# Performance work log

Hardware: AMD Instinct MI355X
Metric: run time of the kernel (lower is better)

## Reference

```python
import jax, jax.numpy as jnp
import numpy as np

V, D, C, B, S, H = 50000, 256, 10, 64, 512, 512


def setup_inputs() -> dict:
    key = jax.random.key(0)
    ks = jax.random.split(key, 12)
    s = 0.02
    return {
        "x": jax.random.randint(ks[0], (B, S), 0, V),
        "embed_w": jax.random.normal(ks[1], (V, D), dtype=jnp.float32) * s,
        "Wl": jax.random.normal(ks[2], (D, D), dtype=jnp.float32) * s,
        "bl": jnp.zeros((D,), jnp.float32),
        "Wsl": jax.random.normal(ks[3], (D, D), dtype=jnp.float32) * s,
        "bsl": jnp.zeros((D,), jnp.float32),
        "Wr": jax.random.normal(ks[4], (D, D), dtype=jnp.float32) * s,
        "br": jnp.zeros((D,), jnp.float32),
        "Wsr": jax.random.normal(ks[5], (D, D), dtype=jnp.float32) * s,
        "bsr": jnp.zeros((D,), jnp.float32),
        "conv_w": jax.random.normal(ks[6], (H, 3 * D), dtype=jnp.float32) * s,
        "conv_b": jnp.zeros((H,), jnp.float32),
        "fc_w": jax.random.normal(ks[7], (C, H), dtype=jnp.float32) * s,
        "fc_b": jnp.zeros((C,), jnp.float32),
        "cl0": jax.random.normal(ks[8], (B, D), dtype=jnp.float32),
        "cr0": jax.random.normal(ks[9], (B, D), dtype=jnp.float32),
    }


def reference(x, embed_w, Wl, bl, Wsl, bsl, Wr, br, Wsr, bsr,
              conv_w, conv_b, fc_w, fc_b, cl0, cr0):
    e = embed_w[x]  # [B,S,D] embedding lookup
    # Precompute the embedding-dependent half of each recurrence (one big GEMM)
    pre_l = jnp.swapaxes(jnp.einsum("bsd,ed->bse", e, Wsl) + bsl, 0, 1)  # [S,B,D]
    pre_r = jnp.swapaxes(jnp.einsum("bsd,ed->bse", e, Wsr) + bsr, 0, 1)  # [S,B,D]

    # left[0]=cl0; left[t]=relu(Wl left[t-1] + Wsl e[t-1])  (output carry, then update)
    def lstep(c, p):
        return jax.nn.relu(c @ Wl.T + bl + p), c

    _, left = jax.lax.scan(lstep, cl0, pre_l)  # [S,B,D]

    # right[S-1]=cr0; right[t]=relu(Wr right[t+1] + Wsr e[t+1])
    def rstep(c, p):
        return jax.nn.relu(c @ Wr.T + br + p), c

    _, right = jax.lax.scan(rstep, cr0, pre_r, reverse=True)  # [S,B,D]

    ctx = jnp.concatenate(
        [jnp.swapaxes(left, 0, 1), e, jnp.swapaxes(right, 0, 1)], axis=-1
    )  # [B,S,3D]
    # Conv2d(1,512,(1,3D)) == per-timestep linear 3D->512
    h = jax.nn.relu(jnp.einsum("bsd,hd->bsh", ctx, conv_w) + conv_b)  # [B,S,H]
    pooled = h.max(axis=1)  # max_pool1d over full sequence -> [B,H]
    return pooled @ fc_w.T + fc_b  # [B,C]
```

## Files before the change

### kernel.cpp

```cpp
#include <hip/hip_runtime.h>
#include <hip/hip_bf16.h>

#define VOCAB 50000
#define DD 256
#define NCLS 10
#define BB 64
#define SS 512
#define HH 512
#define K3D 768

typedef __attribute__((ext_vector_type(8))) short bf16x8;
typedef __attribute__((ext_vector_type(8))) unsigned short ush8;
typedef __attribute__((ext_vector_type(4))) float f32x4;

static __device__ __forceinline__ unsigned short f2bf(float f) {
    __hip_bfloat16 h = __float2bfloat16(f);
    return *reinterpret_cast<unsigned short*>(&h);
}

static __device__ __forceinline__ ush8 cvt8(const float* src) {
    const float4 lo = *(const float4*)(src);
    const float4 hi = *(const float4*)(src + 4);
    uint4 u;
    asm("v_cvt_pk_bf16_f32 %0, %1, %2" : "=v"(u.x) : "v"(lo.x), "v"(lo.y));
    asm("v_cvt_pk_bf16_f32 %0, %1, %2" : "=v"(u.y) : "v"(lo.z), "v"(lo.w));
    asm("v_cvt_pk_bf16_f32 %0, %1, %2" : "=v"(u.z) : "v"(hi.x), "v"(hi.y));
    asm("v_cvt_pk_bf16_f32 %0, %1, %2" : "=v"(u.w) : "v"(hi.z), "v"(hi.w));
    return *reinterpret_cast<ush8*>(&u);
}

#define PPAD 72

__global__ __launch_bounds__(256) void prep_pre_kernel(
    const float* __restrict__ Wsl, const float* __restrict__ Wsr,
    const float* __restrict__ bsl, const float* __restrict__ bl,
    const float* __restrict__ bsr, const float* __restrict__ br,
    const int* __restrict__ x, const float* __restrict__ embed_w,
    const float* __restrict__ conv_w,
    unsigned short* __restrict__ convwb,
    float* __restrict__ pre2_l, float* __restrict__ pre2_r,
    float* __restrict__ pooled)
{
    __shared__ unsigned short Abuf[2][128][PPAD];
    __shared__ unsigned short Bbuf[2][128][PPAD];
    __shared__ int xs[128];

    const int bid = blockIdx.x;
    const int tid = threadIdx.x;

    if (bid < 1024) {
        const int mi  = bid & 3;
        const int sbi = bid >> 2;
        const int w = tid >> 6, lane = tid & 63;
        const int lr = lane & 15, g = lane >> 4;
        const int lk = g * 8;
        const int strow = tid >> 3;
        const int skc   = (tid & 7) * 8;

        if (tid < 128)
            xs[tid] = x[(tid & 63) * SS + 2 * sbi + (tid >> 6)];

        f32x4 acc[2][8];
#pragma unroll
        for (int mt = 0; mt < 2; ++mt)
#pragma unroll
            for (int nt = 0; nt < 8; ++nt) acc[mt][nt] = (f32x4)(0.f);

        auto stage = [&](int ks, int buf) {
            const int k0 = ks * 64;
#pragma unroll
            for (int j = 0; j < 4; ++j) {
                const int row = strow + 32 * j;
                const float* wsrc = (mi < 2 ? Wsl + (size_t)(mi * 128 + row) * DD
                                            : Wsr + (size_t)((mi - 2) * 128 + row) * DD)
                                    + k0 + skc;
                *(ush8*)&Abuf[buf][row][skc] = cvt8(wsrc);
                const float* esrc = embed_w + (size_t)xs[row] * DD + k0 + skc;
                *(ush8*)&Bbuf[buf][row][skc] = cvt8(esrc);
            }
        };

        __syncthreads();
        stage(0, 0);
        int cur = 0;
        for (int ks = 0; ks < 4; ++ks) {
            __syncthreads();
            if (ks + 1 < 4) stage(ks + 1, cur ^ 1);
#pragma unroll
            for (int k2 = 0; k2 < 2; ++k2) {
                const int kk = k2 * 32 + lk;
                const bf16x8 a0 = *(const bf16x8*)&Abuf[cur][w * 32 + lr][kk];
                const bf16x8 a1 = *(const bf16x8*)&Abuf[cur][w * 32 + 16 + lr][kk];
#pragma unroll
                for (int nt = 0; nt < 8; ++nt) {
                    const bf16x8 bv = *(const bf16x8*)&Bbuf[cur][nt * 16 + lr][kk];
                    acc[0][nt] = __builtin_amdgcn_mfma_f32_16x16x32_bf16(a0, bv, acc[0][nt], 0, 0, 0);
                    acc[1][nt] = __builtin_amdgcn_mfma_f32_16x16x32_bf16(a1, bv, acc[1][nt], 0, 0, 0);
                }
            }
            cur ^= 1;
        }

#pragma unroll
        for (int mt = 0; mt < 2; ++mt) {
            const int eg = mi * 128 + w * 32 + mt * 16 + g * 4;
            const int e  = eg & 255;
            const float* bsx = (eg < 256) ? bsl : bsr;
            const float* bbx = (eg < 256) ? bl  : br;
            const float4 b1 = *(const float4*)(bsx + e);
            const float4 b2 = *(const float4*)(bbx + e);
            float* dstb = (eg >= 256) ? pre2_r : pre2_l;
#pragma unroll
            for (int nt = 0; nt < 8; ++nt) {
                const int sb = sbi * 128 + nt * 16 + lr;
                const int s = sb >> 6, bgq = (sb >> 4) & 3, b_loc = sb & 15;
                float4 v;
                v.x = acc[mt][nt][0] + b1.x + b2.x;
                v.y = acc[mt][nt][1] + b1.y + b2.y;
                v.z = acc[mt][nt][2] + b1.z + b2.z;
                v.w = acc[mt][nt][3] + b1.w + b2.w;
                *(float4*)(dstb + ((size_t)s * 4 + bgq) * 4096 + (e >> 2) * 64 + b_loc * 4) = v;
            }
        }
    } else if (bid < 1216) {
        const int g = (bid - 1024) * 256 + tid;
        *(ush8*)(convwb + (size_t)g * 8) = cvt8(conv_w + (size_t)g * 8);
    } else {
        float4* p = (float4*)pooled;
#pragma unroll
        for (int i = 0; i < 32; ++i)
            p[tid + 256 * i] = make_float4(0.f, 0.f, 0.f, 0.f);
    }
}

#define CSWZ(row, off) ((off) ^ (((row) & 15) << 4))
#define APAD 72

__global__ __launch_bounds__(256, 1) void recur_conve_kernel(
    const float* __restrict__ Wl, const float* __restrict__ Wr,
    const float* __restrict__ cl0, const float* __restrict__ cr0,
    const float* __restrict__ pre2_l, const float* __restrict__ pre2_r,
    unsigned short* __restrict__ outl, unsigned short* __restrict__ outr,
    const int* __restrict__ x, const float* __restrict__ embed_w,
    const unsigned short* __restrict__ convwb,
    unsigned short* __restrict__ hpart)
{
    __shared__ alignas(16) unsigned char smem[2 * 2 * 128 * APAD * 2];
    __shared__ int xsv[512];

    const int tid  = threadIdx.x;
    const int lane = tid & 63;

    if (blockIdx.x < 8) {
        unsigned short* cbf0 = (unsigned short*)smem;
        unsigned short* cbf1 = (unsigned short*)smem + 16 * 256;

        const int dir = blockIdx.x >> 2;
        const int bg  = blockIdx.x & 3;
        const int b0  = bg * 16;
        const int wl  = tid >> 6;
        const int col = lane & 15;
        const int g   = lane >> 4;

        const float* W   = dir ? Wr : Wl;
        const float* c0  = dir ? cr0 : cl0;
        const float* pre = dir ? pre2_r : pre2_l;
        unsigned short* out = dir ? outr : outl;

        bf16x8 wfrag[4][8];
#pragma unroll
        for (int mt = 0; mt < 4; ++mt)
#pragma unroll
            for (int i = 0; i < 8; ++i) {
                const int kt = (i + 2 * wl) & 7;
                const float* src = W + (size_t)(wl * 64 + mt * 16 + col) * DD
                                     + kt * 32 + g * 8;
                const ush8 p = cvt8(src);
                wfrag[mt][i] = *(bf16x8*)&p;
            }

        int soff[8];
#pragma unroll
        for (int i = 0; i < 8; ++i) {
            const int kt = (i + 2 * wl) & 7;
            soff[i] = CSWZ(col, kt * 64 + g * 16);
        }

        {
            const int blc = tid >> 4;
            const int ch  = tid & 15;
            const float* src = c0 + (size_t)(b0 + blc) * DD + ch * 16;
            const ush8 p0 = cvt8(src);
            const ush8 p1 = cvt8(src + 8);
            char* rowp = (char*)cbf0 + blc * 512;
            *(ush8*)(rowp + CSWZ(blc, ch * 32))      = p0;
            *(ush8*)(rowp + CSWZ(blc, ch * 32 + 16)) = p1;
            const int t0 = dir ? 511 : 0;
            ush8* dst = (ush8*)(out + ((size_t)t0 * BB + b0 + blc) * DD + ch * 16);
            dst[0] = p0; dst[1] = p1;
        }

        const int lpre = (wl * 16 + g) * 64 + col * 4;
        const ptrdiff_t pstep = dir ? -(ptrdiff_t)16384 : (ptrdiff_t)16384;
        const float* p0 = pre + ((size_t)(dir ? 511 : 0) * 4 + bg) * 4096 + lpre;

        float4 pA0 = *(const float4*)(p0);
        float4 pA1 = *(const float4*)(p0 + 256);
        float4 pA2 = *(const float4*)(p0 + 512);
        float4 pA3 = *(const float4*)(p0 + 768);
        const float* p1p = p0 + pstep;
        float4 pB0 = *(const float4*)(p1p);
        float4 pB1 = *(const float4*)(p1p + 256);
        float4 pB2 = *(const float4*)(p1p + 512);
        float4 pB3 = *(const float4*)(p1p + 768);
        const float* pfetch = p0 + 2 * pstep;

        unsigned short* oplane = out + (size_t)(dir ? 510 : 1) * BB * DD
                                     + (b0 + col) * DD + wl * 64 + g * 4;
        const ptrdiff_t ostep = (dir ? -(ptrdiff_t)1 : (ptrdiff_t)1) * (BB * DD);

        __syncthreads();

        int cur = 0;
#pragma unroll 2
        for (int k = 0; k < SS - 1; ++k) {
            bf16x8 sfrag[8];
            {
                const char* rowp = (const char*)(cur ? cbf1 : cbf0) + col * 512;
#pragma unroll
                for (int i = 0; i < 8; ++i)
                    sfrag[i] = *(const bf16x8*)(rowp + soff[i]);
            }

            const float4 pN0 = *(const float4*)(pfetch);
            const float4 pN1 = *(const float4*)(pfetch + 256);
            const float4 pN2 = *(const float4*)(pfetch + 512);
            const float4 pN3 = *(const float4*)(pfetch + 768);
            if (k < SS - 4) pfetch += pstep;

            char* nbuf = (char*)(cur ? cbf0 : cbf1) + col * 512;

            auto epi = [&](int mt, const f32x4 a) {
                const float v0 = fmaxf(a[0], 0.f);
                const float v1 = fmaxf(a[1], 0.f);
                const float v2 = fmaxf(a[2], 0.f);
                const float v3 = fmaxf(a[3], 0.f);
                uint2 uu;
                asm("v_cvt_pk_bf16_f32 %0, %1, %2" : "=v"(uu.x) : "v"(v0), "v"(v1));
                asm("v_cvt_pk_bf16_f32 %0, %1, %2" : "=v"(uu.y) : "v"(v2), "v"(v3));
                const int eoff = (wl * 64 + mt * 16 + g * 4) * 2;
                *(uint2*)(nbuf + CSWZ(col, eoff)) = uu;
                *(uint2*)(oplane + mt * 16) = uu;
            };

            f32x4 a0 = *(const f32x4*)&pA0;
            f32x4 a1 = *(const f32x4*)&pA1;
            __builtin_amdgcn_s_setprio(1);
#pragma unroll
            for (int i = 0; i < 8; ++i) {
                a0 = __builtin_amdgcn_mfma_f32_16x16x32_bf16(wfrag[0][i], sfrag[i], a0, 0, 0, 0);
                a1 = __builtin_amdgcn_mfma_f32_16x16x32_bf16(wfrag[1][i], sfrag[i], a1, 0, 0, 0);
            }
            __builtin_amdgcn_s_setprio(0);
            epi(0, a0);
            epi(1, a1);

            f32x4 a2 = *(const f32x4*)&pA2;
            f32x4 a3 = *(const f32x4*)&pA3;
            __builtin_amdgcn_s_setprio(1);
#pragma unroll
            for (int i = 0; i < 8; ++i) {
                a2 = __builtin_amdgcn_mfma_f32_16x16x32_bf16(wfrag[2][i], sfrag[i], a2, 0, 0, 0);
                a3 = __builtin_amdgcn_mfma_f32_16x16x32_bf16(wfrag[3][i], sfrag[i], a3, 0, 0, 0);
            }
            __builtin_amdgcn_s_setprio(0);
            epi(2, a2);
            epi(3, a3);

            pA0 = pB0; pA1 = pB1; pA2 = pB2; pA3 = pB3;
            pB0 = pN0; pB1 = pN1; pB2 = pN2; pB3 = pN3;
            oplane += ostep;

            asm volatile("s_waitcnt lgkmcnt(0)" ::: "memory");
            __builtin_amdgcn_s_barrier();
            asm volatile("" ::: "memory");
            cur ^= 1;
        }
        return;
    }

    unsigned short* Ab = (unsigned short*)smem;
    unsigned short* Bb = (unsigned short*)smem + 2 * 128 * APAD;

    const int wid = tid >> 6;
    const int lr  = lane & 15;
    const int lk  = (lane >> 4) * 8;
    const int strow = tid >> 3;
    const int skc   = (tid & 7) * 8;

    for (int rep = 0; rep < 2; ++rep) {
        const int cid = (blockIdx.x - 8) + rep * 128;
        const int b   = cid >> 2;
        const int h0  = (cid & 3) * 128;

        for (int i = tid; i < SS; i += 256) xsv[i] = x[b * SS + i];
        __syncthreads();

        f32x4 acc[2][8];
#pragma unroll
        for (int st = 0; st < 2; ++st)
#pragma unroll
            for (int ht = 0; ht < 8; ++ht) acc[st][ht] = (f32x4)(0.f);

        auto stage = [&](int it, int buf) {
            const int stile = it >> 2, kstep = it & 3;
            const int k0 = kstep * 64;
            const int s0 = stile * 128;
#pragma unroll
            for (int j = 0; j < 4; ++j) {
                const int row = strow + 32 * j;
                const int ss = s0 + row;
                const float* esrc = embed_w + (size_t)xsv[ss] * DD + k0 + skc;
                *(ush8*)&Ab[(buf * 128 + row) * APAD + skc] = cvt8(esrc);
                *(bf16x8*)&Bb[(buf * 128 + row) * APAD + skc] =
                    *(const bf16x8*)(convwb + (size_t)(h0 + row) * K3D + 256 + k0 + skc);
            }
        };

        stage(0, 0);
        int cur = 0;
        for (int it = 0; it < 16; ++it) {
            __syncthreads();
            if (it + 1 < 16) stage(it + 1, cur ^ 1);

            const int wrow0 = wid * 32;
#pragma unroll
            for (int ks = 0; ks < 2; ++ks) {
                const int kk = ks * 32 + lk;
                const bf16x8 a0 = *(const bf16x8*)&Ab[(cur * 128 + wrow0 + lr) * APAD + kk];
                const bf16x8 a1 = *(const bf16x8*)&Ab[(cur * 128 + wrow0 + 16 + lr) * APAD + kk];
#pragma unroll
                for (int ht = 0; ht < 8; ++ht) {
                    const bf16x8 bv = *(const bf16x8*)&Bb[(cur * 128 + ht * 16 + lr) * APAD + kk];
                    acc[0][ht] = __builtin_amdgcn_mfma_f32_16x16x32_bf16(a0, bv, acc[0][ht], 0, 0, 0);
                    acc[1][ht] = __builtin_amdgcn_mfma_f32_16x16x32_bf16(a1, bv, acc[1][ht], 0, 0, 0);
                }
            }
            if ((it & 3) == 3) {
                const int stile = it >> 2;
                unsigned short* hp = hpart + (size_t)(cid * 4 + stile) * 16384;
#pragma unroll
                for (int st = 0; st < 2; ++st)
#pragma unroll
                    for (int ht = 0; ht < 8; ++ht) {
                        uint2 uu;
                        asm("v_cvt_pk_bf16_f32 %0, %1, %2"
                            : "=v"(uu.x) : "v"(acc[st][ht][0]), "v"(acc[st][ht][1]));
                        asm("v_cvt_pk_bf16_f32 %0, %1, %2"
                            : "=v"(uu.y) : "v"(acc[st][ht][2]), "v"(acc[st][ht][3]));
                        const int f = (wid * 2 + st) * 8 + ht;
                        *(uint2*)(hp + f * 256 + lane * 4) = uu;
                        acc[st][ht] = (f32x4)(0.f);
                    }
            }
            cur ^= 1;
        }
        __syncthreads();
    }
}

#define KSTEP 64
#define NKC 8

__global__ __launch_bounds__(256) void conv_pool_kernel(
    const unsigned short* __restrict__ leftb,
    const unsigned short* __restrict__ rightb,
    const unsigned short* __restrict__ convwb,
    const unsigned short* __restrict__ hpart,
    const float* __restrict__ conv_b,
    float* __restrict__ pooled)
{
    __shared__ unsigned short Abuf[2][128][APAD];
    __shared__ unsigned short Bbuf[2][128][APAD];
    __shared__ float red[4][128];

    const int stile = blockIdx.x & 3;
    const int h0i   = (blockIdx.x >> 2) & 3;
    const int b     = blockIdx.x >> 4;
    const int h0    = h0i * 128;
    const int s0    = stile * 128;
    const int tid = threadIdx.x;
    const int wid = tid >> 6;
    const int lane = tid & 63;
    const int lr  = lane & 15;
    const int lk  = (lane >> 4) * 8;
    const int strow = tid >> 3;
    const int skc   = (tid & 7) * 8;

    f32x4 acc[2][8];
    {
        const unsigned short* hp = hpart
            + ((size_t)((b * 4 + h0i) * 4 + stile)) * 16384;
#pragma unroll
        for (int st = 0; st < 2; ++st)
#pragma unroll
            for (int ht = 0; ht < 8; ++ht) {
                const int f = (wid * 2 + st) * 8 + ht;
                const uint2 uu = *(const uint2*)(hp + f * 256 + lane * 4);
                f32x4 v;
                v[0] = __uint_as_float(uu.x << 16);
                v[1] = __uint_as_float(uu.x & 0xffff0000u);
                v[2] = __uint_as_float(uu.y << 16);
                v[3] = __uint_as_float(uu.y & 0xffff0000u);
                acc[st][ht] = v;
            }
    }

    auto stage = [&](int kstep, int buf) {
        const int k0 = kstep * KSTEP;
        const unsigned short* asrc;
        int koff, bcol;
        if (k0 < DD) { asrc = leftb;  koff = k0;      bcol = k0; }
        else         { asrc = rightb; koff = k0 - DD; bcol = k0 + 256; }
#pragma unroll
        for (int j = 0; j < 4; ++j) {
            const int row = strow + 32 * j;
            const int ss = s0 + row;
            *(bf16x8*)&Abuf[buf][row][skc] =
                *(const bf16x8*)(asrc + ((size_t)ss * BB + b) * DD + koff + skc);
            *(bf16x8*)&Bbuf[buf][row][skc] =
                *(const bf16x8*)(convwb + (size_t)(h0 + row) * K3D + bcol + skc);
        }
    };

    stage(0, 0);
    int cur = 0;
    for (int it = 0; it < NKC; ++it) {
        __syncthreads();
        if (it + 1 < NKC) stage(it + 1, cur ^ 1);

        const int wrow0 = wid * 32;
#pragma unroll
        for (int ks = 0; ks < 2; ++ks) {
            const int kk = ks * 32 + lk;
            const bf16x8 a0 = *(const bf16x8*)&Abuf[cur][wrow0 + lr][kk];
            const bf16x8 a1 = *(const bf16x8*)&Abuf[cur][wrow0 + 16 + lr][kk];
#pragma unroll
            for (int ht = 0; ht < 8; ++ht) {
                const bf16x8 bv = *(const bf16x8*)&Bbuf[cur][ht * 16 + lr][kk];
                acc[0][ht] = __builtin_amdgcn_mfma_f32_16x16x32_bf16(a0, bv, acc[0][ht], 0, 0, 0);
                acc[1][ht] = __builtin_amdgcn_mfma_f32_16x16x32_bf16(a1, bv, acc[1][ht], 0, 0, 0);
            }
        }
        cur ^= 1;
    }

    float pmax[8];
#pragma unroll
    for (int ht = 0; ht < 8; ++ht) {
        float m = -INFINITY;
#pragma unroll
        for (int st = 0; st < 2; ++st)
#pragma unroll
            for (int r = 0; r < 4; ++r)
                m = fmaxf(m, acc[st][ht][r]);
        m = fmaxf(m, __shfl_xor(m, 16));
        m = fmaxf(m, __shfl_xor(m, 32));
        if (lane < 16) red[wid][ht * 16 + lane] = m;
    }
    __syncthreads();
    if (tid < 128) {
        const float m = fmaxf(fmaxf(red[0][tid], red[1][tid]),
                              fmaxf(red[2][tid], red[3][tid]));
        const float v = fmaxf(m + conv_b[h0 + tid], 0.f);
        atomicMax((unsigned*)(pooled + (size_t)b * HH + h0 + tid),
                  __float_as_uint(v));
    }
}

__global__ void fc_kernel(const float* __restrict__ pooled,
                          const float* __restrict__ fc_w,
                          const float* __restrict__ fc_b,
                          float* __restrict__ out)
{
    const int t = threadIdx.x;
    if (t >= BB * NCLS) return;
    const int b = t / NCLS, c = t % NCLS;
    float acc = fc_b[c];
    for (int h = 0; h < HH; ++h)
        acc += pooled[(size_t)b * HH + h] * fc_w[(size_t)c * HH + h];
    out[b * NCLS + c] = acc;
}

extern "C" void kernel_launch(void* const* d_in, const int* in_sizes, int n_in,
                              void* d_out, int out_size, void* d_ws, size_t ws_size,
                              hipStream_t stream)
{
    const int*   x       = (const int*)  d_in[0];
    const float* embed_w = (const float*)d_in[1];
    const float* Wl      = (const float*)d_in[2];
    const float* bl      = (const float*)d_in[3];
    const float* Wsl     = (const float*)d_in[4];
    const float* bsl     = (const float*)d_in[5];
    const float* Wr      = (const float*)d_in[6];
    const float* br      = (const float*)d_in[7];
    const float* Wsr     = (const float*)d_in[8];
    const float* bsr     = (const float*)d_in[9];
    const float* conv_w  = (const float*)d_in[10];
    const float* conv_b  = (const float*)d_in[11];
    const float* fc_w    = (const float*)d_in[12];
    const float* fc_b    = (const float*)d_in[13];
    const float* cl0     = (const float*)d_in[14];
    const float* cr0     = (const float*)d_in[15];
    float* out = (float*)d_out;

    char* ws = (char*)d_ws;
    const size_t SZf = (size_t)SS * BB * DD * sizeof(float);
    const size_t SZh = (size_t)SS * BB * DD * sizeof(unsigned short);
    float*          pre2_l = (float*)(ws);
    float*          pre2_r = (float*)(ws + SZf);
    unsigned short* leftb  = (unsigned short*)(ws + 2 * SZf);
    unsigned short* rightb = (unsigned short*)(ws + 2 * SZf + SZh);
    unsigned short* convwb = (unsigned short*)(ws + 2 * SZf + 2 * SZh);
    float*          pooled = (float*)(ws + 2 * SZf + 2 * SZh + (size_t)HH * K3D * 2);
    unsigned short* hpart  = (unsigned short*)(ws + 2 * SZf + 2 * SZh
                                               + (size_t)HH * K3D * 2
                                               + (size_t)BB * HH * 4);

    prep_pre_kernel<<<1217, 256, 0, stream>>>(
        Wsl, Wsr, bsl, bl, bsr, br, x, embed_w, conv_w,
        convwb, pre2_l, pre2_r, pooled);

    recur_conve_kernel<<<136, 256, 0, stream>>>(
        Wl, Wr, cl0, cr0, pre2_l, pre2_r, leftb, rightb,
        x, embed_w, convwb, hpart);

    conv_pool_kernel<<<1024, 256, 0, stream>>>(
        leftb, rightb, convwb, hpart, conv_b, pooled);

    fc_kernel<<<1, BB * NCLS, 0, stream>>>(pooled, fc_w, fc_b, out);
}
```

Baseline: 426.0 us.

## Overlap pre-activation GEMM with recurrence using per-timestep readiness counters

Moves the embedding-projection GEMM into the same launch as the recurrence. GEMM blocks publish completion through per-step atomic counters and are ordered from both sequence ends, so each recurrence block can start as soon as its next timesteps are ready instead of waiting for the whole GEMM kernel. The aim is to hide the GEMM time and one kernel boundary behind the serial recurrence. The cost is spin-waiting on global atomics, which relies on the recurrence blocks (low block indices) being scheduled alongside the GEMM blocks and risks stalls if block dispatch order is not guaranteed.

```diff
diff --git a/kernel.cpp b/kernel.cpp
--- a/kernel.cpp
+++ b/kernel.cpp
@@ -29,123 +29,43 @@
     return *reinterpret_cast<ush8*>(&u);
 }
 
-#define PPAD 72
-
-__global__ __launch_bounds__(256) void prep_pre_kernel(
+__global__ __launch_bounds__(256) void prep_small_kernel(
+    const float* __restrict__ conv_w,
+    unsigned short* __restrict__ convwb,
+    float* __restrict__ pooled,
+    int* __restrict__ cnt)
+{
+    const int bid = blockIdx.x;
+    const int tid = threadIdx.x;
+    if (bid < 192) {
+        const int g = bid * 256 + tid;
+        *(ush8*)(convwb + (size_t)g * 8) = cvt8(conv_w + (size_t)g * 8);
+    } else {
+        float4* p = (float4*)pooled;
+#pragma unroll
+        for (int i = 0; i < 32; ++i)
+            p[tid + 256 * i] = make_float4(0.f, 0.f, 0.f, 0.f);
+        if (tid < 128) ((int4*)cnt)[tid] = make_int4(0, 0, 0, 0);
+    }
+}
+
+#define CSWZ(row, off) ((off) ^ (((row) & 15) << 4))
+#define APAD 72
+
+__global__ __launch_bounds__(256, 1) void recur_pre_conve_kernel(
+    const float* __restrict__ Wl, const float* __restrict__ Wr,
+    const float* __restrict__ cl0, const float* __restrict__ cr0,
     const float* __restrict__ Wsl, const float* __restrict__ Wsr,
     const float* __restrict__ bsl, const float* __restrict__ bl,
     const float* __restrict__ bsr, const float* __restrict__ br,
     const int* __restrict__ x, const float* __restrict__ embed_w,
-    const float* __restrict__ conv_w,
-    unsigned short* __restrict__ convwb,
     float* __restrict__ pre2_l, float* __restrict__ pre2_r,
-    float* __restrict__ pooled)
+    unsigned short* __restrict__ outl, unsigned short* __restrict__ outr,
+    const unsigned short* __restrict__ convwb,
+    unsigned short* __restrict__ hpart,
+    int* __restrict__ cnt)
 {
-    __shared__ unsigned short Abuf[2][128][PPAD];
-    __shared__ unsigned short Bbuf[2][128][PPAD];
-    __shared__ int xs[128];
-
-    const int bid = blockIdx.x;
-    const int tid = threadIdx.x;
-
-    if (bid < 1024) {
-        const int mi  = bid & 3;
-        const int sbi = bid >> 2;
-        const int w = tid >> 6, lane = tid & 63;
-        const int lr = lane & 15, g = lane >> 4;
-        const int lk = g * 8;
-        const int strow = tid >> 3;
-        const int skc   = (tid & 7) * 8;
-
-        if (tid < 128)
-            xs[tid] = x[(tid & 63) * SS + 2 * sbi + (tid >> 6)];
-
-        f32x4 acc[2][8];
-#pragma unroll
-        for (int mt = 0; mt < 2; ++mt)
-#pragma unroll
-            for (int nt = 0; nt < 8; ++nt) acc[mt][nt] = (f32x4)(0.f);
-
-        auto stage = [&](int ks, int buf) {
-            const int k0 = ks * 64;
-#pragma unroll
-            for (int j = 0; j < 4; ++j) {
-                const int row = strow + 32 * j;
-                const float* wsrc = (mi < 2 ? Wsl + (size_t)(mi * 128 + row) * DD
-                                            : Wsr + (size_t)((mi - 2) * 128 + row) * DD)
-                                    + k0 + skc;
-                *(ush8*)&Abuf[buf][row][skc] = cvt8(wsrc);
-                const float* esrc = embed_w + (size_t)xs[row] * DD + k0 + skc;
-                *(ush8*)&Bbuf[buf][row][skc] = cvt8(esrc);
-            }
-        };
-
-        __syncthreads();
-        stage(0, 0);
-        int cur = 0;
-        for (int ks = 0; ks < 4; ++ks) {
-            __syncthreads();
-            if (ks + 1 < 4) stage(ks + 1, cur ^ 1);
-#pragma unroll
-            for (int k2 = 0; k2 < 2; ++k2) {
-                const int kk = k2 * 32 + lk;
-                const bf16x8 a0 = *(const bf16x8*)&Abuf[cur][w * 32 + lr][kk];
-                const bf16x8 a1 = *(const bf16x8*)&Abuf[cur][w * 32 + 16 + lr][kk];
-#pragma unroll
-                for (int nt = 0; nt < 8; ++nt) {
-                    const bf16x8 bv = *(const bf16x8*)&Bbuf[cur][nt * 16 + lr][kk];
-                    acc[0][nt] = __builtin_amdgcn_mfma_f32_16x16x32_bf16(a0, bv, acc[0][nt], 0, 0, 0);
-                    acc[1][nt] = __builtin_amdgcn_mfma_f32_16x16x32_bf16(a1, bv, acc[1][nt], 0, 0, 0);
-                }
-            }
-            cur ^= 1;
-        }
-
-#pragma unroll
-        for (int mt = 0; mt < 2; ++mt) {
-            const int eg = mi * 128 + w * 32 + mt * 16 + g * 4;
-            const int e  = eg & 255;
-            const float* bsx = (eg < 256) ? bsl : bsr;
-            const float* bbx = (eg < 256) ? bl  : br;
-            const float4 b1 = *(const float4*)(bsx + e);
-            const float4 b2 = *(const float4*)(bbx + e);
-            float* dstb = (eg >= 256) ? pre2_r : pre2_l;
-#pragma unroll
-            for (int nt = 0; nt < 8; ++nt) {
-                const int sb = sbi * 128 + nt * 16 + lr;
-                const int s = sb >> 6, bgq = (sb >> 4) & 3, b_loc = sb & 15;
-                float4 v;
-                v.x = acc[mt][nt][0] + b1.x + b2.x;
-                v.y = acc[mt][nt][1] + b1.y + b2.y;
-                v.z = acc[mt][nt][2] + b1.z + b2.z;
-                v.w = acc[mt][nt][3] + b1.w + b2.w;
-                *(float4*)(dstb + ((size_t)s * 4 + bgq) * 4096 + (e >> 2) * 64 + b_loc * 4) = v;
-            }
-        }
-    } else if (bid < 1216) {
-        const int g = (bid - 1024) * 256 + tid;
-        *(ush8*)(convwb + (size_t)g * 8) = cvt8(conv_w + (size_t)g * 8);
-    } else {
-        float4* p = (float4*)pooled;
-#pragma unroll
-        for (int i = 0; i < 32; ++i)
-            p[tid + 256 * i] = make_float4(0.f, 0.f, 0.f, 0.f);
-    }
-}
-
-#define CSWZ(row, off) ((off) ^ (((row) & 15) << 4))
-#define APAD 72
-
-__global__ __launch_bounds__(256, 1) void recur_conve_kernel(
-    const float* __restrict__ Wl, const float* __restrict__ Wr,
-    const float* __restrict__ cl0, const float* __restrict__ cr0,
-    const float* __restrict__ pre2_l, const float* __restrict__ pre2_r,
-    unsigned short* __restrict__ outl, unsigned short* __restrict__ outr,
-    const int* __restrict__ x, const float* __restrict__ embed_w,
-    const unsigned short* __restrict__ convwb,
-    unsigned short* __restrict__ hpart)
-{
-    __shared__ alignas(16) unsigned char smem[2 * 2 * 128 * APAD * 2];
+    __shared__ alignas(16) unsigned char smem[82048];
     __shared__ int xsv[512];
 
     const int tid  = threadIdx.x;
@@ -166,6 +86,31 @@
         const float* c0  = dir ? cr0 : cl0;
         const float* pre = dir ? pre2_r : pre2_l;
         unsigned short* out = dir ? outr : outl;
+        int* cbase = cnt + dir * 256;
+
+        int wm = 0;
+        auto cover = [&](int sNeed) {
+            const int sq = sNeed >> 1;
+            if (dir == 0) {
+                while (wm <= sq) {
+                    int c = 0;
+                    if (lane == 0)
+                        c = __hip_atomic_load(cbase + wm, __ATOMIC_ACQUIRE,
+                                              __HIP_MEMORY_SCOPE_AGENT);
+                    c = __shfl(c, 0);
+                    if (c == 2) ++wm;
+                }
+            } else {
+                while (wm < 256 - sq) {
+                    int c = 0;
+                    if (lane == 0)
+                        c = __hip_atomic_load(cbase + (255 - wm), __ATOMIC_ACQUIRE,
+                                              __HIP_MEMORY_SCOPE_AGENT);
+                    c = __shfl(c, 0);
+                    if (c == 2) ++wm;
+                }
+            }
+        };
 
         bf16x8 wfrag[4][8];
 #pragma unroll
@@ -204,6 +149,8 @@
         const ptrdiff_t pstep = dir ? -(ptrdiff_t)16384 : (ptrdiff_t)16384;
         const float* p0 = pre + ((size_t)(dir ? 511 : 0) * 4 + bg) * 4096 + lpre;
 
+        cover(dir ? 510 : 1);
+
         float4 pA0 = *(const float4*)(p0);
         float4 pA1 = *(const float4*)(p0 + 256);
         float4 pA2 = *(const float4*)(p0 + 512);
@@ -232,6 +179,11 @@
                     sfrag[i] = *(const bf16x8*)(rowp + soff[i]);
             }
 
+            {
+                int sN = dir ? (509 - k) : (k + 2);
+                sN = (sN < 1) ? 1 : (sN > 510 ? 510 : sN);
+                cover(sN);
+            }
             const float4 pN0 = *(const float4*)(pfetch);
             const float4 pN1 = *(const float4*)(pfetch + 256);
             const float4 pN2 = *(const float4*)(pfetch + 512);
@@ -289,6 +241,95 @@
         return;
     }
 
+    if (blockIdx.x < 1032) {
+        unsigned short (*Abuf)[128][APAD] = (unsigned short (*)[128][APAD])smem;
+        unsigned short (*Bbuf)[128][APAD] =
+            (unsigned short (*)[128][APAD])(smem + 2 * 128 * APAD * 2);
+
+        const int j  = blockIdx.x - 8;
+        const int pb = j >> 2;
+        const int mi = j & 3;
+        const int sbi = (pb & 1) ? 255 - (pb >> 1) : (pb >> 1);
+
+        const int w = tid >> 6;
+        const int lr = lane & 15, g = lane >> 4;
+        const int lk = g * 8;
+        const int strow = tid >> 3;
+        const int skc   = (tid & 7) * 8;
+
+        if (tid < 128)
+            xsv[tid] = x[(tid & 63) * SS + 2 * sbi + (tid >> 6)];
+
+        f32x4 acc[2][8];
+#pragma unroll
+        for (int mt = 0; mt < 2; ++mt)
+#pragma unroll
+            for (int nt = 0; nt < 8; ++nt) acc[mt][nt] = (f32x4)(0.f);
+
+        auto stage = [&](int ks, int buf) {
+            const int k0 = ks * 64;
+#pragma unroll
+            for (int jj = 0; jj < 4; ++jj) {
+                const int row = strow + 32 * jj;
+                const float* wsrc = (mi < 2 ? Wsl + (size_t)(mi * 128 + row) * DD
+                                            : Wsr + (size_t)((mi - 2) * 128 + row) * DD)
+                                    + k0 + skc;
+                *(ush8*)&Abuf[buf][row][skc] = cvt8(wsrc);
+                const float* esrc = embed_w + (size_t)xsv[row] * DD + k0 + skc;
+                *(ush8*)&Bbuf[buf][row][skc] = cvt8(esrc);
+            }
+        };
+
+        __syncthreads();
+        stage(0, 0);
+        int cur = 0;
+        for (int ks = 0; ks < 4; ++ks) {
+            __syncthreads();
+            if (ks + 1 < 4) stage(ks + 1, cur ^ 1);
+#pragma unroll
+            for (int k2 = 0; k2 < 2; ++k2) {
+                const int kk = k2 * 32 + lk;
+                const bf16x8 a0 = *(const bf16x8*)&Abuf[cur][w * 32 + lr][kk];
+                const bf16x8 a1 = *(const bf16x8*)&Abuf[cur][w * 32 + 16 + lr][kk];
+#pragma unroll
+                for (int nt = 0; nt < 8; ++nt) {
+                    const bf16x8 bv = *(const bf16x8*)&Bbuf[cur][nt * 16 + lr][kk];
+                    acc[0][nt] = __builtin_amdgcn_mfma_f32_16x16x32_bf16(a0, bv, acc[0][nt], 0, 0, 0);
+                    acc[1][nt] = __builtin_amdgcn_mfma_f32_16x16x32_bf16(a1, bv, acc[1][nt], 0, 0, 0);
+                }
+            }
+            cur ^= 1;
+        }
+
+#pragma unroll
+        for (int mt = 0; mt < 2; ++mt) {
+            const int eg = mi * 128 + w * 32 + mt * 16 + g * 4;
+            const int e  = eg & 255;
+            const float* bsx = (eg < 256) ? bsl : bsr;
+            const float* bbx = (eg < 256) ? bl  : br;
+            const float4 b1 = *(const float4*)(bsx + e);
+            const float4 b2 = *(const float4*)(bbx + e);
+            float* dstb = (eg >= 256) ? pre2_r : pre2_l;
+#pragma unroll
+            for (int nt = 0; nt < 8; ++nt) {
+                const int sb = sbi * 128 + nt * 16 + lr;
+                const int s = sb >> 6, bgq = (sb >> 4) & 3, b_loc = sb & 15;
+                float4 v;
+                v.x = acc[mt][nt][0] + b1.x + b2.x;
+                v.y = acc[mt][nt][1] + b1.y + b2.y;
+                v.z = acc[mt][nt][2] + b1.z + b2.z;
+                v.w = acc[mt][nt][3] + b1.w + b2.w;
+                *(float4*)(dstb + ((size_t)s * 4 + bgq) * 4096 + (e >> 2) * 64 + b_loc * 4) = v;
+            }
+        }
+
+        __syncthreads();
+        if (tid == 0)
+            __hip_atomic_fetch_add(cnt + (mi >> 1) * 256 + sbi, 1,
+                                   __ATOMIC_RELEASE, __HIP_MEMORY_SCOPE_AGENT);
+        return;
+    }
+
     unsigned short* Ab = (unsigned short*)smem;
     unsigned short* Bb = (unsigned short*)smem + 2 * 128 * APAD;
 
@@ -299,7 +340,7 @@
     const int skc   = (tid & 7) * 8;
 
     for (int rep = 0; rep < 2; ++rep) {
-        const int cid = (blockIdx.x - 8) + rep * 128;
+        const int cid = (blockIdx.x - 1032) + rep * 128;
         const int b   = cid >> 2;
         const int h0  = (cid & 3) * 128;
 
@@ -317,8 +358,8 @@
             const int k0 = kstep * 64;
             const int s0 = stile * 128;
 #pragma unroll
-            for (int j = 0; j < 4; ++j) {
-                const int row = strow + 32 * j;
+            for (int jj = 0; jj < 4; ++jj) {
+                const int row = strow + 32 * jj;
                 const int ss = s0 + row;
                 const float* esrc = embed_w + (size_t)xsv[ss] * DD + k0 + skc;
                 *(ush8*)&Ab[(buf * 128 + row) * APAD + skc] = cvt8(esrc);
@@ -526,14 +567,16 @@
     unsigned short* hpart  = (unsigned short*)(ws + 2 * SZf + 2 * SZh
                                                + (size_t)HH * K3D * 2
                                                + (size_t)BB * HH * 4);
-
-    prep_pre_kernel<<<1217, 256, 0, stream>>>(
-        Wsl, Wsr, bsl, bl, bsr, br, x, embed_w, conv_w,
-        convwb, pre2_l, pre2_r, pooled);
-
-    recur_conve_kernel<<<136, 256, 0, stream>>>(
-        Wl, Wr, cl0, cr0, pre2_l, pre2_r, leftb, rightb,
-        x, embed_w, convwb, hpart);
+    int*            cnt    = (int*)(ws + 2 * SZf + 2 * SZh
+                                    + (size_t)HH * K3D * 2
+                                    + (size_t)BB * HH * 4
+                                    + (size_t)1024 * 16384 * 2);
+
+    prep_small_kernel<<<193, 256, 0, stream>>>(conv_w, convwb, pooled, cnt);
+
+    recur_pre_conve_kernel<<<1160, 256, 0, stream>>>(
+        Wl, Wr, cl0, cr0, Wsl, Wsr, bsl, bl, bsr, br, x, embed_w,
+        pre2_l, pre2_r, leftb, rightb, convwb, hpart, cnt);
 
     conv_pool_kernel<<<1024, 256, 0, stream>>>(
         leftb, rightb, convwb, hpart, conv_b, pooled);
```

New measurement: 546.6 us. 1.28x slower.
